# Kernel optimization log

Hardware: AMD Instinct MI355X
Metric: run time of the kernel (lower is better)

Reference implementation:

```python
import jax, jax.numpy as jnp
import numpy as np

DIM = 1024
N_HEADS = 16
HEAD_DIM = DIM // N_HEADS


def setup_inputs() -> dict:
    key = jax.random.key(0)
    ks = jax.random.split(key, 5)
    B, L = 2, 2048
    q = jax.random.normal(ks[0], (B, L, DIM), dtype=jnp.float32)
    # nn.Linear weights: shape [out_features, in_features], applied as x @ W.T
    scale = 1.0 / np.sqrt(DIM)
    Wq = jax.random.normal(ks[1], (DIM, DIM), dtype=jnp.float32) * scale
    Wk = jax.random.normal(ks[2], (DIM, DIM), dtype=jnp.float32) * scale
    Wv = jax.random.normal(ks[3], (DIM, DIM), dtype=jnp.float32) * scale
    Wo = jax.random.normal(ks[4], (DIM, DIM), dtype=jnp.float32) * scale
    return {"q": q, "Wq": Wq, "Wk": Wk, "Wv": Wv, "Wo": Wo}


def reference(q, Wq, Wk, Wv, Wo):
    B, L, _ = q.shape
    kv = q  # self-attention (kv=None path)
    # projections: x @ W.T, then split heads: b l (h d) -> b h l d
    def split_heads(x):
        return x.reshape(B, L, N_HEADS, HEAD_DIM).transpose(0, 2, 1, 3)
    qh = split_heads(q @ Wq.T)
    kh = split_heads(kv @ Wk.T)
    vh = split_heads(kv @ Wv.T)
    # scaled dot-product attention; scale = sqrt(head_dim)
    scores = jnp.einsum('bhid,bhjd->bhij', qh, kh) / jnp.sqrt(
        jnp.asarray(HEAD_DIM, dtype=qh.dtype))
    attn = jax.nn.softmax(scores, axis=-1)
    out = jnp.einsum('bhij,bhjd->bhid', attn, vh)
    # b h l d -> b l (h d)
    out = out.transpose(0, 2, 1, 3).reshape(B, L, DIM)
    return out @ Wo.T
```

## Files before the change

### kernel.cpp

```cpp
#include <hip/hip_runtime.h>


#define DIMN 1024
#define NH 16
#define HD 64
#define BB 2
#define LL 2048

typedef float f32x4 __attribute__((ext_vector_type(4)));
typedef short s16x8 __attribute__((ext_vector_type(8)));

#define QSCALE 0.18033688011112042f

static __device__ __forceinline__ unsigned short f2bf(float f) {
  unsigned u = __float_as_uint(f);
  u += 0x7fffu + ((u >> 16) & 1u);
  return (unsigned short)(u >> 16);
}
static __device__ __forceinline__ unsigned packbf2(float lo, float hi) {
  return (unsigned)f2bf(lo) | ((unsigned)f2bf(hi) << 16);
}
static __device__ __forceinline__ float xexp2(float x) {
#if __has_builtin(__builtin_amdgcn_exp2f)
  return __builtin_amdgcn_exp2f(x);
#else
  return exp2f(x);
#endif
}
static __device__ __forceinline__ s16x8 cvt8(float4 a, float4 b) {
  s16x8 r;
  r[0] = (short)f2bf(a.x); r[1] = (short)f2bf(a.y);
  r[2] = (short)f2bf(a.z); r[3] = (short)f2bf(a.w);
  r[4] = (short)f2bf(b.x); r[5] = (short)f2bf(b.y);
  r[6] = (short)f2bf(b.z); r[7] = (short)f2bf(b.w);
  return r;
}
static __device__ __forceinline__ void gld16(const unsigned short* g,
                                             unsigned short* l) {
#if __has_builtin(__builtin_amdgcn_global_load_lds)
  __builtin_amdgcn_global_load_lds(
      (const __attribute__((address_space(1))) void*)g,
      (__attribute__((address_space(3))) void*)l, 16, 0, 0);
#else
  ((uint4*)l)[threadIdx.x & 63] = ((const uint4*)g)[0];
#endif
}

static __device__ __forceinline__ int vpos(int s128) {
  return (s128 & 0x60) | ((s128 & 0x0C) << 1) | ((s128 & 0x10) >> 2) | (s128 & 3);
}

__global__ __launch_bounds__(256) void cvt_all(
    const float* __restrict__ X, const float* __restrict__ Wq,
    const float* __restrict__ Wk, const float* __restrict__ Wv,
    const float* __restrict__ Wo, unsigned short* __restrict__ out) {
  const int blk = blockIdx.x;
  const float* src;
  unsigned short* dst;
  size_t off;
  if (blk < 2048) {
    src = X; dst = out; off = (size_t)blk * 2048;
  } else {
    int s = (blk - 2048) >> 9;
    src = (s == 0) ? Wq : (s == 1) ? Wk : (s == 2) ? Wv : Wo;
    dst = out + ((size_t)1 << 22) + (size_t)s * (1u << 20);
    off = (size_t)((blk - 2048) & 511) * 2048;
  }
  size_t i = off + (size_t)threadIdx.x * 8;
  float4 v0 = *(const float4*)(src + i);
  float4 v1 = *(const float4*)(src + i + 4);
  uint4 o;
  o.x = packbf2(v0.x, v0.y); o.y = packbf2(v0.z, v0.w);
  o.z = packbf2(v1.x, v1.y); o.w = packbf2(v1.z, v1.w);
  *(uint4*)(dst + i) = o;
}

__global__ __launch_bounds__(256) void gemm_qkv(
    const unsigned short* __restrict__ Xb, const unsigned short* __restrict__ Wb,
    unsigned short* __restrict__ Qb, unsigned short* __restrict__ Kb,
    unsigned short* __restrict__ VT) {
  __shared__ __align__(16) unsigned short Al[128 * 64];
  __shared__ __align__(16) unsigned short Bl[128 * 64];
  const int lin = blockIdx.x;
  const int xcd = lin & 7, sblk = lin >> 3;
  const int m0 = ((xcd & 3) * 8 + (sblk & 7)) * 128;
  const int n0g = ((xcd >> 2) * 12 + (sblk >> 3)) * 128;
  const int sel = n0g >> 10;
  const int tid = threadIdx.x;
  const int w = tid >> 6, lane = tid & 63;
  const int c = lane & 15, quad = lane >> 4;
  const int wm = (w & 1) * 64, wn = (w >> 1) * 64;

  f32x4 zero = {0.f, 0.f, 0.f, 0.f};
  f32x4 acc[4][4];
#pragma unroll
  for (int i = 0; i < 4; ++i)
#pragma unroll
    for (int j = 0; j < 4; ++j) acc[i][j] = zero;

  const int l8 = lane >> 3, p8 = lane & 7;
  const unsigned short* gA = Xb + (size_t)(m0 + w * 8 + l8) * DIMN + ((p8 ^ l8) * 8);
  const unsigned short* gB = Wb + (size_t)(n0g + w * 8 + l8) * DIMN + ((p8 ^ l8) * 8);
  unsigned short* lA = Al + (w * 8) * 64;
  unsigned short* lB = Bl + (w * 8) * 64;
  const int c7 = c & 7;

  for (int k0 = 0; k0 < DIMN; k0 += 64) {
    __syncthreads();
#pragma unroll
    for (int r = 0; r < 4; ++r) {
      gld16(gA + k0 + (size_t)(r * 32) * DIMN, lA + r * 32 * 64);
      gld16(gB + k0 + (size_t)(r * 32) * DIMN, lB + r * 32 * 64);
    }
    __syncthreads();
#pragma unroll
    for (int f = 0; f < 2; ++f) {
      const int rd = ((f * 4 + quad) ^ c7) * 8;
      s16x8 a[4], b[4];
#pragma unroll
      for (int i = 0; i < 4; ++i)
        a[i] = *(const s16x8*)&Al[(wm + i * 16 + c) * 64 + rd];
#pragma unroll
      for (int j = 0; j < 4; ++j)
        b[j] = *(const s16x8*)&Bl[(wn + j * 16 + c) * 64 + rd];
      if (sel != 2) {
#pragma unroll
        for (int i = 0; i < 4; ++i)
#pragma unroll
          for (int j = 0; j < 4; ++j)
            acc[i][j] = __builtin_amdgcn_mfma_f32_16x16x32_bf16(b[j], a[i], acc[i][j], 0, 0, 0);
      } else {
#pragma unroll
        for (int i = 0; i < 4; ++i)
#pragma unroll
          for (int j = 0; j < 4; ++j)
            acc[i][j] = __builtin_amdgcn_mfma_f32_16x16x32_bf16(a[i], b[j], acc[i][j], 0, 0, 0);
      }
    }
  }

  const int n0 = n0g & 1023;
  if (sel != 2) {
    unsigned short* Out = (sel == 0) ? Qb : Kb;
    const float scale = (sel == 0) ? QSCALE : 1.0f;
    const int bi = (m0 + wm) >> 11;
#pragma unroll
    for (int i = 0; i < 4; ++i) {
      const int li = (m0 + wm + i * 16 + c) & 2047;
#pragma unroll
      for (int j = 0; j < 4; ++j) {
        const int nq = n0 + wn + j * 16 + quad * 4;
        const int h = nq >> 6, d = nq & 63;
        uint2 st;
        st.x = packbf2(acc[i][j][0] * scale, acc[i][j][1] * scale);
        st.y = packbf2(acc[i][j][2] * scale, acc[i][j][3] * scale);
        *(uint2*)&Out[(((size_t)bi * NH + h) * LL + li) * HD + d] = st;
      }
    }
  } else {
    const int bi = m0 >> 11;
    const int mlo = m0 & 2047;
#pragma unroll
    for (int i = 0; i < 4; ++i) {
      const int pos = mlo + vpos(wm + i * 16 + quad * 4);
#pragma unroll
      for (int j = 0; j < 4; ++j) {
        const int nv = n0 + wn + j * 16 + c;
        const int h = nv >> 6, d = nv & 63;
        uint2 st;
        st.x = packbf2(acc[i][j][0], acc[i][j][1]);
        st.y = packbf2(acc[i][j][2], acc[i][j][3]);
        *(uint2*)&VT[(((size_t)bi * NH + h) * HD + d) * LL + pos] = st;
      }
    }
  }
}

__global__ __launch_bounds__(256) void gemm_o(
    const unsigned short* __restrict__ A, const unsigned short* __restrict__ Wob,
    float* __restrict__ Out) {
  __shared__ __align__(16) unsigned short Al[128 * 64];
  __shared__ __align__(16) unsigned short Bl[64 * 64];
  const int lin = blockIdx.x;
  const int xcd = lin & 7, sblk = lin >> 3;
  const int m0 = ((sblk >> 4) * 8 + xcd) * 128;
  const int n0 = (sblk & 15) * 64;
  const int tid = threadIdx.x;
  const int w = tid >> 6, lane = tid & 63;
  const int c = lane & 15, quad = lane >> 4;
  const int wm = (w & 1) * 64, wn = (w >> 1) * 32;

  f32x4 zero = {0.f, 0.f, 0.f, 0.f};
  f32x4 acc[4][2];
#pragma unroll
  for (int i = 0; i < 4; ++i)
#pragma unroll
    for (int j = 0; j < 2; ++j) acc[i][j] = zero;

  const int l8 = lane >> 3, p8 = lane & 7;
  const unsigned short* gA = A + (size_t)(m0 + w * 8 + l8) * DIMN + ((p8 ^ l8) * 8);
  const unsigned short* gB = Wob + (size_t)(n0 + w * 8 + l8) * DIMN + ((p8 ^ l8) * 8);
  unsigned short* lA = Al + (w * 8) * 64;
  unsigned short* lB = Bl + (w * 8) * 64;
  const int c7 = c & 7;

  for (int k0 = 0; k0 < DIMN; k0 += 64) {
    __syncthreads();
#pragma unroll
    for (int r = 0; r < 4; ++r)
      gld16(gA + k0 + (size_t)(r * 32) * DIMN, lA + r * 32 * 64);
#pragma unroll
    for (int r = 0; r < 2; ++r)
      gld16(gB + k0 + (size_t)(r * 32) * DIMN, lB + r * 32 * 64);
    __syncthreads();
#pragma unroll
    for (int f = 0; f < 2; ++f) {
      const int rd = ((f * 4 + quad) ^ c7) * 8;
      s16x8 a[4], b[2];
#pragma unroll
      for (int i = 0; i < 4; ++i)
        a[i] = *(const s16x8*)&Al[(wm + i * 16 + c) * 64 + rd];
#pragma unroll
      for (int j = 0; j < 2; ++j)
        b[j] = *(const s16x8*)&Bl[(wn + j * 16 + c) * 64 + rd];
#pragma unroll
      for (int i = 0; i < 4; ++i)
#pragma unroll
        for (int j = 0; j < 2; ++j)
          acc[i][j] = __builtin_amdgcn_mfma_f32_16x16x32_bf16(a[i], b[j], acc[i][j], 0, 0, 0);
    }
  }

#pragma unroll
  for (int i = 0; i < 4; ++i)
#pragma unroll
    for (int j = 0; j < 2; ++j)
#pragma unroll
      for (int r = 0; r < 4; ++r)
        Out[(size_t)(m0 + wm + i * 16 + quad * 4 + r) * DIMN + n0 + wn + j * 16 + c] =
            acc[i][j][r];
}

__global__ __launch_bounds__(512, 4) void attn9(
    const unsigned short* __restrict__ Qb, const unsigned short* __restrict__ Kb,
    const unsigned short* __restrict__ VT, unsigned short* __restrict__ AO) {
  __shared__ __align__(16) unsigned short Kl[2][2][64 * 64];
  __shared__ __align__(16) unsigned short Vtl[2][2][64 * 64];

  const int lin = blockIdx.x;
  const int xcd = lin & 7, sblk = lin >> 3;
  const int bh = (sblk >> 4) * 8 + xcd;
  const int qi = sblk & 15;
  const int tid = threadIdx.x;
  const int w = tid >> 6, lane = tid & 63;
  const int half = w >> 2, wl = w & 3;
  const int c = lane & 15, quad = lane >> 4;
  const int qa = qi * 128 + wl * 16;
  const int qbr = qa + 64;

  const unsigned short* Qh = Qb + (size_t)bh * LL * HD;
  const unsigned short* Kh = Kb + (size_t)bh * LL * HD + (size_t)half * 1024 * HD;
  const unsigned short* Vh = VT + (size_t)bh * HD * LL + half * 1024;

  s16x8 qA0 = *(const s16x8*)(Qh + (size_t)(qa + c) * HD + quad * 8);
  s16x8 qA1 = *(const s16x8*)(Qh + (size_t)(qa + c) * HD + 32 + quad * 8);
  s16x8 qB0 = *(const s16x8*)(Qh + (size_t)(qbr + c) * HD + quad * 8);
  s16x8 qB1 = *(const s16x8*)(Qh + (size_t)(qbr + c) * HD + 32 + quad * 8);

  f32x4 zero = {0.f, 0.f, 0.f, 0.f};
  f32x4 oA[4], oB[4];
  float lsumA = 0.f, lsumB = 0.f;
#pragma unroll
  for (int dc = 0; dc < 4; ++dc) { oA[dc] = zero; oB[dc] = zero; }

  const int l8 = lane >> 3, p8 = lane & 7;
  const unsigned short* gK = Kh + (size_t)(wl * 16 + l8) * HD + ((p8 ^ l8) * 8);
  const int vr = wl * 16 + l8;
  const unsigned short* gV = Vh + (size_t)vr * LL + ((p8 ^ l8) * 8);

  const int c7 = c & 7;
  const int kpa = (quad ^ c7) * 8;
  const int kpb = ((quad + 4) ^ c7) * 8;

#define STAGE(buf, kv)                                                        \
  do {                                                                        \
    unsigned short* lK_ = &Kl[half][buf][(wl * 16) * 64];                     \
    unsigned short* lV_ = &Vtl[half][buf][(wl * 16) * 64];                    \
    gld16(gK + (size_t)(kv) * HD, lK_);                                       \
    gld16(gK + (size_t)((kv) + 8) * HD, lK_ + 8 * 64);                        \
    gld16(gV + (kv), lV_);                                                    \
    gld16(gV + (size_t)8 * LL + (kv), lV_ + 8 * 64);                          \
  } while (0)

  STAGE(0, 0);

  for (int it = 0; it < 16; ++it) {
    __syncthreads();
    if (it + 1 < 16) STAGE((it + 1) & 1, (it + 1) * 64);
    const unsigned short* Kt = &Kl[half][it & 1][0];
    const unsigned short* Vt = &Vtl[half][it & 1][0];

    f32x4 sA[4], sB[4];
#pragma unroll
    for (int t4 = 0; t4 < 4; ++t4) {
      const unsigned short* kr = Kt + (t4 * 16 + c) * 64;
      s16x8 kfa = *(const s16x8*)(kr + kpa);
      s16x8 kfb = *(const s16x8*)(kr + kpb);
      sA[t4] = __builtin_amdgcn_mfma_f32_16x16x32_bf16(kfa, qA0, zero, 0, 0, 0);
      sA[t4] = __builtin_amdgcn_mfma_f32_16x16x32_bf16(kfb, qA1, sA[t4], 0, 0, 0);
      sB[t4] = __builtin_amdgcn_mfma_f32_16x16x32_bf16(kfa, qB0, zero, 0, 0, 0);
      sB[t4] = __builtin_amdgcn_mfma_f32_16x16x32_bf16(kfb, qB1, sB[t4], 0, 0, 0);
    }

    float pA[4][4], pB[4][4];
    float a0 = 0.f, a1 = 0.f, b0 = 0.f, b1 = 0.f;
#pragma unroll
    for (int t4 = 0; t4 < 4; ++t4)
#pragma unroll
      for (int r = 0; r < 4; ++r) {
        float eA = xexp2(sA[t4][r]);
        float eB = xexp2(sB[t4][r]);
        pA[t4][r] = eA; pB[t4][r] = eB;
        if (t4 & 1) { a1 += eA; b1 += eB; } else { a0 += eA; b0 += eB; }
      }
    lsumA += a0 + a1; lsumB += b0 + b1;

    s16x8 pfA[2], pfB[2];
#pragma unroll
    for (int kh = 0; kh < 2; ++kh) {
      unsigned puA[4], puB[4];
      puA[0] = __builtin_amdgcn_perm(__float_as_uint(pA[2 * kh][1]),
                                     __float_as_uint(pA[2 * kh][0]), 0x07060302u);
      puA[1] = __builtin_amdgcn_perm(__float_as_uint(pA[2 * kh][3]),
                                     __float_as_uint(pA[2 * kh][2]), 0x07060302u);
      puA[2] = __builtin_amdgcn_perm(__float_as_uint(pA[2 * kh + 1][1]),
                                     __float_as_uint(pA[2 * kh + 1][0]), 0x07060302u);
      puA[3] = __builtin_amdgcn_perm(__float_as_uint(pA[2 * kh + 1][3]),
                                     __float_as_uint(pA[2 * kh + 1][2]), 0x07060302u);
      puB[0] = __builtin_amdgcn_perm(__float_as_uint(pB[2 * kh][1]),
                                     __float_as_uint(pB[2 * kh][0]), 0x07060302u);
      puB[1] = __builtin_amdgcn_perm(__float_as_uint(pB[2 * kh][3]),
                                     __float_as_uint(pB[2 * kh][2]), 0x07060302u);
      puB[2] = __builtin_amdgcn_perm(__float_as_uint(pB[2 * kh + 1][1]),
                                     __float_as_uint(pB[2 * kh + 1][0]), 0x07060302u);
      puB[3] = __builtin_amdgcn_perm(__float_as_uint(pB[2 * kh + 1][3]),
                                     __float_as_uint(pB[2 * kh + 1][2]), 0x07060302u);
      pfA[kh] = *(const s16x8*)puA;
      pfB[kh] = *(const s16x8*)puB;
    }

#pragma unroll
    for (int kh = 0; kh < 2; ++kh) {
#pragma unroll
      for (int dc = 0; dc < 4; ++dc) {
        s16x8 vf = *(const s16x8*)(Vt + (dc * 16 + c) * 64 +
                                   (((kh * 4 + quad) ^ c7) * 8));
        oA[dc] = __builtin_amdgcn_mfma_f32_16x16x32_bf16(vf, pfA[kh], oA[dc], 0, 0, 0);
        oB[dc] = __builtin_amdgcn_mfma_f32_16x16x32_bf16(vf, pfB[kh], oB[dc], 0, 0, 0);
      }
    }
  }
#undef STAGE

  float lA = lsumA;
  lA += __shfl_xor(lA, 16);
  lA += __shfl_xor(lA, 32);
  float lB = lsumB;
  lB += __shfl_xor(lB, 16);
  lB += __shfl_xor(lB, 32);

  f32x4* ob4 = (f32x4*)&Kl[0][0][0];
  float* lb = (float*)&Vtl[0][0][0];

  __syncthreads();
  if (half == 1) {
#pragma unroll
    for (int dc = 0; dc < 4; ++dc) {
      ob4[((wl * 2 + 0) * 4 + dc) * 64 + lane] = oA[dc];
      ob4[((wl * 2 + 1) * 4 + dc) * 64 + lane] = oB[dc];
    }
    lb[(wl * 2 + 0) * 64 + lane] = lA;
    lb[(wl * 2 + 1) * 64 + lane] = lB;
  }
  __syncthreads();
  if (half == 0) {
    lA += lb[(wl * 2 + 0) * 64 + lane];
    lB += lb[(wl * 2 + 1) * 64 + lane];
    float invA = 1.0f / lA;
    float invB = 1.0f / lB;
    const int bi = bh >> 4, h = bh & 15;
    unsigned short* dstA = AO + ((size_t)bi * LL + qa + c) * DIMN + h * HD + quad * 4;
    unsigned short* dstB = AO + ((size_t)bi * LL + qbr + c) * DIMN + h * HD + quad * 4;
#pragma unroll
    for (int dc = 0; dc < 4; ++dc) {
      f32x4 sa = oA[dc] + ob4[((wl * 2 + 0) * 4 + dc) * 64 + lane];
      f32x4 sb = oB[dc] + ob4[((wl * 2 + 1) * 4 + dc) * 64 + lane];
      uint2 stA, stB;
      stA.x = packbf2(sa[0] * invA, sa[1] * invA);
      stA.y = packbf2(sa[2] * invA, sa[3] * invA);
      stB.x = packbf2(sb[0] * invB, sb[1] * invB);
      stB.y = packbf2(sb[2] * invB, sb[3] * invB);
      *(uint2*)(dstA + dc * 16) = stA;
      *(uint2*)(dstB + dc * 16) = stB;
    }
  }
}

__global__ __launch_bounds__(64) void qkv_proj_f(
    const float* __restrict__ X, const float* __restrict__ Wq,
    const float* __restrict__ Wk, const float* __restrict__ Wv,
    unsigned short* __restrict__ Qb, unsigned short* __restrict__ Kb,
    unsigned short* __restrict__ VT) {
  const int m0 = blockIdx.x * 64;
  const int n0g = blockIdx.y * 64;
  const int sel = n0g >> 10;
  const int n0 = n0g & 1023;
  const float* W = (sel == 0) ? Wq : (sel == 1) ? Wk : Wv;
  const int lane = threadIdx.x;
  const int c = lane & 15, quad = lane >> 4;

  f32x4 zero = {0.f, 0.f, 0.f, 0.f};
  f32x4 acc[4][4];
#pragma unroll
  for (int i = 0; i < 4; ++i)
#pragma unroll
    for (int j = 0; j < 4; ++j) acc[i][j] = zero;

  const float* ab = X + (size_t)(m0 + c) * DIMN + quad * 8;
  const float* bb = W + (size_t)(n0 + c) * DIMN + quad * 8;

  for (int k0 = 0; k0 < DIMN; k0 += 32) {
    s16x8 a[4], b[4];
#pragma unroll
    for (int i = 0; i < 4; ++i) {
      const float* pp = ab + i * 16 * DIMN + k0;
      a[i] = cvt8(*(const float4*)pp, *(const float4*)(pp + 4));
    }
#pragma unroll
    for (int j = 0; j < 4; ++j) {
      const float* pp = bb + j * 16 * DIMN + k0;
      b[j] = cvt8(*(const float4*)pp, *(const float4*)(pp + 4));
    }
    if (sel != 2) {
#pragma unroll
      for (int i = 0; i < 4; ++i)
#pragma unroll
        for (int j = 0; j < 4; ++j)
          acc[i][j] = __builtin_amdgcn_mfma_f32_16x16x32_bf16(a[i], b[j], acc[i][j], 0, 0, 0);
    } else {
#pragma unroll
      for (int i = 0; i < 4; ++i)
#pragma unroll
        for (int j = 0; j < 4; ++j)
          acc[i][j] = __builtin_amdgcn_mfma_f32_16x16x32_bf16(b[j], a[i], acc[i][j], 0, 0, 0);
    }
  }

  if (sel != 2) {
    unsigned short* Out = (sel == 0) ? Qb : Kb;
    const float scale = (sel == 0) ? QSCALE : 1.0f;
#pragma unroll
    for (int i = 0; i < 4; ++i)
#pragma unroll
      for (int j = 0; j < 4; ++j)
#pragma unroll
        for (int r = 0; r < 4; ++r) {
          int row = m0 + i * 16 + quad * 4 + r;
          int nl = n0 + j * 16 + c;
          int bi = row >> 11, li = row & 2047;
          int h = nl >> 6, d = nl & 63;
          Out[(((size_t)bi * NH + h) * LL + li) * HD + d] = f2bf(acc[i][j][r] * scale);
        }
  } else {
#pragma unroll
    for (int i = 0; i < 4; ++i) {
#pragma unroll
      for (int j = 0; j < 4; ++j)
#pragma unroll
        for (int r = 0; r < 4; ++r) {
          int n = n0 + j * 16 + quad * 4 + r;
          int s128 = (m0 & 64) + i * 16 + c;
          int m = (m0 & ~127) + vpos(s128);
          int h = n >> 6, d = n & 63;
          int bi = m0 >> 11;
          VT[(((size_t)bi * NH + h) * HD + d) * LL + (m & 2047)] = f2bf(acc[i][j][r]);
        }
    }
  }
}

__global__ __launch_bounds__(64) void o_proj_f(
    const unsigned short* __restrict__ A, const float* __restrict__ Wo,
    float* __restrict__ Out) {
  const int m0 = blockIdx.x * 64, n0 = blockIdx.y * 64;
  const int lane = threadIdx.x;
  const int c = lane & 15, quad = lane >> 4;

  f32x4 zero = {0.f, 0.f, 0.f, 0.f};
  f32x4 acc[4][4];
#pragma unroll
  for (int i = 0; i < 4; ++i)
#pragma unroll
    for (int j = 0; j < 4; ++j) acc[i][j] = zero;

  const unsigned short* ab = A + (size_t)(m0 + c) * DIMN + quad * 8;
  const float* bb = Wo + (size_t)(n0 + c) * DIMN + quad * 8;

  for (int k0 = 0; k0 < DIMN; k0 += 32) {
    s16x8 a[4], b[4];
#pragma unroll
    for (int i = 0; i < 4; ++i) a[i] = *(const s16x8*)(ab + i * 16 * DIMN + k0);
#pragma unroll
    for (int j = 0; j < 4; ++j) {
      const float* pp = bb + j * 16 * DIMN + k0;
      b[j] = cvt8(*(const float4*)pp, *(const float4*)(pp + 4));
    }
#pragma unroll
    for (int i = 0; i < 4; ++i)
#pragma unroll
      for (int j = 0; j < 4; ++j)
        acc[i][j] = __builtin_amdgcn_mfma_f32_16x16x32_bf16(a[i], b[j], acc[i][j], 0, 0, 0);
  }

#pragma unroll
  for (int i = 0; i < 4; ++i)
#pragma unroll
    for (int j = 0; j < 4; ++j)
#pragma unroll
      for (int r = 0; r < 4; ++r)
        Out[(size_t)(m0 + i * 16 + quad * 4 + r) * DIMN + n0 + j * 16 + c] = acc[i][j][r];
}

extern "C" void kernel_launch(void* const* d_in, const int* in_sizes, int n_in,
                              void* d_out, int out_size, void* d_ws, size_t ws_size,
                              hipStream_t stream) {
  const float* X = (const float*)d_in[0];
  const float* Wq = (const float*)d_in[1];
  const float* Wk = (const float*)d_in[2];
  const float* Wv = (const float*)d_in[3];
  const float* Wo = (const float*)d_in[4];
  float* Out = (float*)d_out;

  const size_t M1 = (size_t)1 << 20;
  unsigned short* ws16 = (unsigned short*)d_ws;

  if (ws_size >= (size_t)48 * 1024 * 1024) {
    unsigned short* Xb = ws16;
    unsigned short* Wb = ws16 + 4 * M1;
    unsigned short* Qb = ws16 + 8 * M1;
    unsigned short* Kb = ws16 + 12 * M1;
    unsigned short* VT = ws16 + 16 * M1;
    unsigned short* AO = ws16 + 20 * M1;
    cvt_all<<<4096, 256, 0, stream>>>(X, Wq, Wk, Wv, Wo, ws16);
    gemm_qkv<<<768, 256, 0, stream>>>(Xb, Wb, Qb, Kb, VT);
    attn9<<<512, 512, 0, stream>>>(Qb, Kb, VT, AO);
    gemm_o<<<512, 256, 0, stream>>>(AO, Wb + 3 * M1, Out);
  } else {
    unsigned short* Qb = ws16;
    unsigned short* Kb = ws16 + 4 * M1;
    unsigned short* VT = ws16 + 8 * M1;
    unsigned short* AO = ws16 + 12 * M1;
    qkv_proj_f<<<dim3(64, 48), 64, 0, stream>>>(X, Wq, Wk, Wv, Qb, Kb, VT);
    attn9<<<512, 512, 0, stream>>>(Qb, Kb, VT, AO);
    o_proj_f<<<dim3(64, 16), 64, 0, stream>>>(AO, Wo, Out);
  }
}
```

Before: 176.4 us.

## Process four query subtiles per wave in attention to reuse K/V fragments

The attention kernel now gives each wave four 16-row query subtiles instead of two, so one block covers 256 query rows and the grid shrinks from 512 to 256 blocks. Each K fragment read from LDS, and each V fragment, now feeds twice as many MFMAs, which halves K/V staging traffic and LDS reads per query. The cross-half reduction of partial outputs is done in two passes through the same shared buffers. In exchange, register use rises (16 output accumulators per wave), the occupancy hint is dropped, and only one block per CU is launched, which leaves less parallelism to hide latency.

```diff
diff --git a/kernel.cpp b/kernel.cpp
--- a/kernel.cpp
+++ b/kernel.cpp
@@ -241,7 +241,7 @@
             acc[i][j][r];
 }
 
-__global__ __launch_bounds__(512, 4) void attn9(
+__global__ __launch_bounds__(512) void attn10(
     const unsigned short* __restrict__ Qb, const unsigned short* __restrict__ Kb,
     const unsigned short* __restrict__ VT, unsigned short* __restrict__ AO) {
   __shared__ __align__(16) unsigned short Kl[2][2][64 * 64];
@@ -249,29 +249,32 @@
 
   const int lin = blockIdx.x;
   const int xcd = lin & 7, sblk = lin >> 3;
-  const int bh = (sblk >> 4) * 8 + xcd;
-  const int qi = sblk & 15;
+  const int bh = (sblk >> 3) * 8 + xcd;
+  const int qblk = sblk & 7;
   const int tid = threadIdx.x;
   const int w = tid >> 6, lane = tid & 63;
   const int half = w >> 2, wl = w & 3;
   const int c = lane & 15, quad = lane >> 4;
-  const int qa = qi * 128 + wl * 16;
-  const int qbr = qa + 64;
+  const int q0 = qblk * 256 + wl * 16;
 
   const unsigned short* Qh = Qb + (size_t)bh * LL * HD;
   const unsigned short* Kh = Kb + (size_t)bh * LL * HD + (size_t)half * 1024 * HD;
   const unsigned short* Vh = VT + (size_t)bh * HD * LL + half * 1024;
 
-  s16x8 qA0 = *(const s16x8*)(Qh + (size_t)(qa + c) * HD + quad * 8);
-  s16x8 qA1 = *(const s16x8*)(Qh + (size_t)(qa + c) * HD + 32 + quad * 8);
-  s16x8 qB0 = *(const s16x8*)(Qh + (size_t)(qbr + c) * HD + quad * 8);
-  s16x8 qB1 = *(const s16x8*)(Qh + (size_t)(qbr + c) * HD + 32 + quad * 8);
+  s16x8 qf[4][2];
+#pragma unroll
+  for (int s = 0; s < 4; ++s) {
+    qf[s][0] = *(const s16x8*)(Qh + (size_t)(q0 + s * 64 + c) * HD + quad * 8);
+    qf[s][1] = *(const s16x8*)(Qh + (size_t)(q0 + s * 64 + c) * HD + 32 + quad * 8);
+  }
 
   f32x4 zero = {0.f, 0.f, 0.f, 0.f};
-  f32x4 oA[4], oB[4];
-  float lsumA = 0.f, lsumB = 0.f;
-#pragma unroll
-  for (int dc = 0; dc < 4; ++dc) { oA[dc] = zero; oB[dc] = zero; }
+  f32x4 o[4][4];
+  float lsum[4] = {0.f, 0.f, 0.f, 0.f};
+#pragma unroll
+  for (int s = 0; s < 4; ++s)
+#pragma unroll
+    for (int dc = 0; dc < 4; ++dc) o[s][dc] = zero;
 
   const int l8 = lane >> 3, p8 = lane & 7;
   const unsigned short* gK = Kh + (size_t)(wl * 16 + l8) * HD + ((p8 ^ l8) * 8);
@@ -300,53 +303,47 @@
     const unsigned short* Kt = &Kl[half][it & 1][0];
     const unsigned short* Vt = &Vtl[half][it & 1][0];
 
-    f32x4 sA[4], sB[4];
+    s16x8 kf[4][2];
 #pragma unroll
     for (int t4 = 0; t4 < 4; ++t4) {
       const unsigned short* kr = Kt + (t4 * 16 + c) * 64;
-      s16x8 kfa = *(const s16x8*)(kr + kpa);
-      s16x8 kfb = *(const s16x8*)(kr + kpb);
-      sA[t4] = __builtin_amdgcn_mfma_f32_16x16x32_bf16(kfa, qA0, zero, 0, 0, 0);
-      sA[t4] = __builtin_amdgcn_mfma_f32_16x16x32_bf16(kfb, qA1, sA[t4], 0, 0, 0);
-      sB[t4] = __builtin_amdgcn_mfma_f32_16x16x32_bf16(kfa, qB0, zero, 0, 0, 0);
-      sB[t4] = __builtin_amdgcn_mfma_f32_16x16x32_bf16(kfb, qB1, sB[t4], 0, 0, 0);
-    }
-
-    float pA[4][4], pB[4][4];
-    float a0 = 0.f, a1 = 0.f, b0 = 0.f, b1 = 0.f;
-#pragma unroll
-    for (int t4 = 0; t4 < 4; ++t4)
-#pragma unroll
-      for (int r = 0; r < 4; ++r) {
-        float eA = xexp2(sA[t4][r]);
-        float eB = xexp2(sB[t4][r]);
-        pA[t4][r] = eA; pB[t4][r] = eB;
-        if (t4 & 1) { a1 += eA; b1 += eB; } else { a0 += eA; b0 += eB; }
-      }
-    lsumA += a0 + a1; lsumB += b0 + b1;
-
-    s16x8 pfA[2], pfB[2];
-#pragma unroll
-    for (int kh = 0; kh < 2; ++kh) {
-      unsigned puA[4], puB[4];
-      puA[0] = __builtin_amdgcn_perm(__float_as_uint(pA[2 * kh][1]),
-                                     __float_as_uint(pA[2 * kh][0]), 0x07060302u);
-      puA[1] = __builtin_amdgcn_perm(__float_as_uint(pA[2 * kh][3]),
-                                     __float_as_uint(pA[2 * kh][2]), 0x07060302u);
-      puA[2] = __builtin_amdgcn_perm(__float_as_uint(pA[2 * kh + 1][1]),
-                                     __float_as_uint(pA[2 * kh + 1][0]), 0x07060302u);
-      puA[3] = __builtin_amdgcn_perm(__float_as_uint(pA[2 * kh + 1][3]),
-                                     __float_as_uint(pA[2 * kh + 1][2]), 0x07060302u);
-      puB[0] = __builtin_amdgcn_perm(__float_as_uint(pB[2 * kh][1]),
-                                     __float_as_uint(pB[2 * kh][0]), 0x07060302u);
-      puB[1] = __builtin_amdgcn_perm(__float_as_uint(pB[2 * kh][3]),
-                                     __float_as_uint(pB[2 * kh][2]), 0x07060302u);
-      puB[2] = __builtin_amdgcn_perm(__float_as_uint(pB[2 * kh + 1][1]),
-                                     __float_as_uint(pB[2 * kh + 1][0]), 0x07060302u);
-      puB[3] = __builtin_amdgcn_perm(__float_as_uint(pB[2 * kh + 1][3]),
-                                     __float_as_uint(pB[2 * kh + 1][2]), 0x07060302u);
-      pfA[kh] = *(const s16x8*)puA;
-      pfB[kh] = *(const s16x8*)puB;
+      kf[t4][0] = *(const s16x8*)(kr + kpa);
+      kf[t4][1] = *(const s16x8*)(kr + kpb);
+    }
+
+    s16x8 pf[4][2];
+#pragma unroll
+    for (int s = 0; s < 4; ++s) {
+      f32x4 sc[4];
+#pragma unroll
+      for (int t4 = 0; t4 < 4; ++t4) {
+        sc[t4] = __builtin_amdgcn_mfma_f32_16x16x32_bf16(kf[t4][0], qf[s][0], zero, 0, 0, 0);
+        sc[t4] = __builtin_amdgcn_mfma_f32_16x16x32_bf16(kf[t4][1], qf[s][1], sc[t4], 0, 0, 0);
+      }
+      float p[4][4];
+      float a0 = 0.f, a1 = 0.f;
+#pragma unroll
+      for (int t4 = 0; t4 < 4; ++t4)
+#pragma unroll
+        for (int r = 0; r < 4; ++r) {
+          float e = xexp2(sc[t4][r]);
+          p[t4][r] = e;
+          if (t4 & 1) a1 += e; else a0 += e;
+        }
+      lsum[s] += a0 + a1;
+#pragma unroll
+      for (int kh = 0; kh < 2; ++kh) {
+        unsigned pu[4];
+        pu[0] = __builtin_amdgcn_perm(__float_as_uint(p[2 * kh][1]),
+                                      __float_as_uint(p[2 * kh][0]), 0x07060302u);
+        pu[1] = __builtin_amdgcn_perm(__float_as_uint(p[2 * kh][3]),
+                                      __float_as_uint(p[2 * kh][2]), 0x07060302u);
+        pu[2] = __builtin_amdgcn_perm(__float_as_uint(p[2 * kh + 1][1]),
+                                      __float_as_uint(p[2 * kh + 1][0]), 0x07060302u);
+        pu[3] = __builtin_amdgcn_perm(__float_as_uint(p[2 * kh + 1][3]),
+                                      __float_as_uint(p[2 * kh + 1][2]), 0x07060302u);
+        pf[s][kh] = *(const s16x8*)pu;
+      }
     }
 
 #pragma unroll
@@ -355,53 +352,55 @@
       for (int dc = 0; dc < 4; ++dc) {
         s16x8 vf = *(const s16x8*)(Vt + (dc * 16 + c) * 64 +
                                    (((kh * 4 + quad) ^ c7) * 8));
-        oA[dc] = __builtin_amdgcn_mfma_f32_16x16x32_bf16(vf, pfA[kh], oA[dc], 0, 0, 0);
-        oB[dc] = __builtin_amdgcn_mfma_f32_16x16x32_bf16(vf, pfB[kh], oB[dc], 0, 0, 0);
+#pragma unroll
+        for (int s = 0; s < 4; ++s)
+          o[s][dc] = __builtin_amdgcn_mfma_f32_16x16x32_bf16(vf, pf[s][kh], o[s][dc], 0, 0, 0);
       }
     }
   }
 #undef STAGE
 
-  float lA = lsumA;
-  lA += __shfl_xor(lA, 16);
-  lA += __shfl_xor(lA, 32);
-  float lB = lsumB;
-  lB += __shfl_xor(lB, 16);
-  lB += __shfl_xor(lB, 32);
+#pragma unroll
+  for (int s = 0; s < 4; ++s) {
+    lsum[s] += __shfl_xor(lsum[s], 16);
+    lsum[s] += __shfl_xor(lsum[s], 32);
+  }
 
   f32x4* ob4 = (f32x4*)&Kl[0][0][0];
   float* lb = (float*)&Vtl[0][0][0];
-
-  __syncthreads();
-  if (half == 1) {
-#pragma unroll
-    for (int dc = 0; dc < 4; ++dc) {
-      ob4[((wl * 2 + 0) * 4 + dc) * 64 + lane] = oA[dc];
-      ob4[((wl * 2 + 1) * 4 + dc) * 64 + lane] = oB[dc];
-    }
-    lb[(wl * 2 + 0) * 64 + lane] = lA;
-    lb[(wl * 2 + 1) * 64 + lane] = lB;
-  }
-  __syncthreads();
-  if (half == 0) {
-    lA += lb[(wl * 2 + 0) * 64 + lane];
-    lB += lb[(wl * 2 + 1) * 64 + lane];
-    float invA = 1.0f / lA;
-    float invB = 1.0f / lB;
-    const int bi = bh >> 4, h = bh & 15;
-    unsigned short* dstA = AO + ((size_t)bi * LL + qa + c) * DIMN + h * HD + quad * 4;
-    unsigned short* dstB = AO + ((size_t)bi * LL + qbr + c) * DIMN + h * HD + quad * 4;
-#pragma unroll
-    for (int dc = 0; dc < 4; ++dc) {
-      f32x4 sa = oA[dc] + ob4[((wl * 2 + 0) * 4 + dc) * 64 + lane];
-      f32x4 sb = oB[dc] + ob4[((wl * 2 + 1) * 4 + dc) * 64 + lane];
-      uint2 stA, stB;
-      stA.x = packbf2(sa[0] * invA, sa[1] * invA);
-      stA.y = packbf2(sa[2] * invA, sa[3] * invA);
-      stB.x = packbf2(sb[0] * invB, sb[1] * invB);
-      stB.y = packbf2(sb[2] * invB, sb[3] * invB);
-      *(uint2*)(dstA + dc * 16) = stA;
-      *(uint2*)(dstB + dc * 16) = stB;
+  const int bi = bh >> 4, h = bh & 15;
+
+#pragma unroll
+  for (int pass = 0; pass < 2; ++pass) {
+    __syncthreads();
+    if (half == 1) {
+#pragma unroll
+      for (int sp = 0; sp < 2; ++sp) {
+        const int s = pass * 2 + sp;
+#pragma unroll
+        for (int dc = 0; dc < 4; ++dc)
+          ob4[((wl * 2 + sp) * 4 + dc) * 64 + lane] = o[s][dc];
+        lb[(wl * 2 + sp) * 64 + lane] = lsum[s];
+      }
+    }
+    __syncthreads();
+    if (half == 0) {
+#pragma unroll
+      for (int sp = 0; sp < 2; ++sp) {
+        const int s = pass * 2 + sp;
+        const float l = lsum[s] + lb[(wl * 2 + sp) * 64 + lane];
+        const float inv = 1.0f / l;
+        unsigned short* dst =
+            AO + ((size_t)bi * LL + q0 + s * 64 + c) * DIMN + h * HD + quad * 4;
+#pragma unroll
+        for (int dc = 0; dc < 4; ++dc) {
+          f32x4 sum = o[s][dc] + ob4[((wl * 2 + sp) * 4 + dc) * 64 + lane];
+          uint2 st;
+          st.x = packbf2(sum[0] * inv, sum[1] * inv);
+          st.y = packbf2(sum[2] * inv, sum[3] * inv);
+          *(uint2*)(dst + dc * 16) = st;
+        }
+      }
     }
   }
 }
@@ -553,7 +552,7 @@
     unsigned short* AO = ws16 + 20 * M1;
     cvt_all<<<4096, 256, 0, stream>>>(X, Wq, Wk, Wv, Wo, ws16);
     gemm_qkv<<<768, 256, 0, stream>>>(Xb, Wb, Qb, Kb, VT);
-    attn9<<<512, 512, 0, stream>>>(Qb, Kb, VT, AO);
+    attn10<<<256, 512, 0, stream>>>(Qb, Kb, VT, AO);
     gemm_o<<<512, 256, 0, stream>>>(AO, Wb + 3 * M1, Out);
   } else {
     unsigned short* Qb = ws16;
@@ -561,7 +560,7 @@
     unsigned short* VT = ws16 + 8 * M1;
     unsigned short* AO = ws16 + 12 * M1;
     qkv_proj_f<<<dim3(64, 48), 64, 0, stream>>>(X, Wq, Wk, Wv, Qb, Kb, VT);
-    attn9<<<512, 512, 0, stream>>>(Qb, Kb, VT, AO);
+    attn10<<<256, 512, 0, stream>>>(Qb, Kb, VT, AO);
     o_proj_f<<<dim3(64, 16), 64, 0, stream>>>(AO, Wo, Out);
   }
 }
```

Measured after the change: 175.3 us. Within noise of the previous version (-0.6%).
